# Kernel optimization log

Measured on AMD Instinct MI355X. Metric: run time of the kernel, lower is better.

Reference implementation:

```python
import jax, jax.numpy as jnp
import numpy as np

N = 100000
E = 1600000
IN_C, HID_C, OUT_C = 128, 128, 64


def setup_inputs() -> dict:
    key = jax.random.key(0)
    ks = jax.random.split(key, 8)
    x = jax.random.normal(ks[0], (N, IN_C), dtype=jnp.float32)
    edge_index = jax.random.randint(ks[1], (2, E), 0, N, dtype=jnp.int64)

    def glorot(k, fan_in, fan_out):
        s = jnp.sqrt(6.0 / (fan_in + fan_out))
        return jax.random.uniform(k, (fan_in, fan_out), jnp.float32, -s, s)

    W1 = glorot(ks[2], IN_C, HID_C)
    b1 = jnp.zeros((HID_C,), jnp.float32)
    W2 = glorot(ks[3], HID_C, HID_C)
    b2 = jnp.zeros((HID_C,), jnp.float32)
    W3 = glorot(ks[4], HID_C, OUT_C)
    b3 = jnp.zeros((OUT_C,), jnp.float32)
    return {"x": x, "edge_index": edge_index,
            "W1": W1, "b1": b1, "W2": W2, "b2": b2, "W3": W3, "b3": b3}


def _gcn_norm(row, col, n_nodes):
    # symmetric normalization, add_self_loops=False (PyG gcn_norm)
    deg = jax.ops.segment_sum(jnp.ones(row.shape[0], jnp.float32), col, num_segments=n_nodes)
    dinv = jnp.where(deg > 0, jax.lax.rsqrt(jnp.maximum(deg, 1.0)), 0.0)
    dinv = jnp.where(deg > 0, deg ** -0.5, 0.0)
    return dinv[row] * dinv[col]  # [E]


def _gcn_conv(x, row, col, norm, W, b):
    h = x @ W                                # [N, F_out] dense GEMM first (PyG order)
    msg = h[row] * norm[:, None]             # gather + scale, [E, F_out]
    out = jax.ops.segment_sum(msg, col, num_segments=x.shape[0])  # scatter-add
    return out + b


def reference(x, edge_index, W1, b1, W2, b2, W3, b3):
    row, col = edge_index[0], edge_index[1]
    norm = _gcn_norm(row, col, x.shape[0])
    h = jax.nn.relu(_gcn_conv(x, row, col, norm, W1, b1))   # dropout is identity in eval
    h = jax.nn.relu(_gcn_conv(h, row, col, norm, W2, b2))
    out = _gcn_conv(h, row, col, norm, W3, b3)
    return out
```

## Files before the change

kernel.cpp:

```cpp
#include <hip/hip_runtime.h>
#include <hip/hip_bf16.h>
#include <hip/hip_fp16.h>


#define K_DIM 128
#define SCAN_CHUNK 1024

typedef _Float16 f16x8 __attribute__((ext_vector_type(8)));
typedef float f32x4 __attribute__((ext_vector_type(4)));
struct h2s { _Float16 x, y; };

static inline long long cdiv_ll(long long a, long long b) { return (a + b - 1) / b; }

__global__ __launch_bounds__(256) void count_kernel(const int* __restrict__ col, int* __restrict__ cnt,
                                                    int* __restrict__ rank, int E) {
    int e = blockIdx.x * 256 + threadIdx.x;
    if (e < E) rank[e] = atomicAdd(&cnt[col[e]], 1);
}

__global__ __launch_bounds__(256) void dinv_kernel(const int* __restrict__ cnt, float* __restrict__ dinv, int N) {
    int n = blockIdx.x * 256 + threadIdx.x;
    if (n < N) {
        int d = cnt[n];
        dinv[n] = (d > 0) ? (1.0f / sqrtf((float)d)) : 0.0f;
    }
}

__global__ __launch_bounds__(256) void scan1_kernel(const int* __restrict__ cnt, int* __restrict__ off,
                                                    int* __restrict__ bsum, int N) {
    __shared__ int lds[256];
    const int t = threadIdx.x;
    const int base = blockIdx.x * SCAN_CHUNK;
    int v[4], s = 0;
#pragma unroll
    for (int j = 0; j < 4; ++j) {
        int i = base + t * 4 + j;
        v[j] = (i < N) ? cnt[i] : 0;
        s += v[j];
    }
    lds[t] = s;
    __syncthreads();
    for (int d = 1; d < 256; d <<= 1) {
        int x = (t >= d) ? lds[t - d] : 0;
        __syncthreads();
        lds[t] += x;
        __syncthreads();
    }
    int excl = lds[t] - s;
    if (t == 255) bsum[blockIdx.x] = lds[255];
    int run = excl;
#pragma unroll
    for (int j = 0; j < 4; ++j) {
        int i = base + t * 4 + j;
        if (i < N) off[i] = run;
        run += v[j];
    }
}

__global__ __launch_bounds__(256) void scan2_kernel(int* __restrict__ bsum, int G, int* __restrict__ off,
                                                    int N, int E) {
    __shared__ int lds[256];
    const int t = threadIdx.x;
    int s = (t < G) ? bsum[t] : 0;
    lds[t] = s;
    __syncthreads();
    for (int d = 1; d < 256; d <<= 1) {
        int x = (t >= d) ? lds[t - d] : 0;
        __syncthreads();
        lds[t] += x;
        __syncthreads();
    }
    if (t < G) bsum[t] = lds[t] - s;
    if (t == 0) off[N] = E;
}

__global__ __launch_bounds__(256) void scan3_kernel(int* __restrict__ off, const int* __restrict__ bsum, int N) {
    int add = bsum[blockIdx.x];
    const int base = blockIdx.x * SCAN_CHUNK;
#pragma unroll
    for (int j = 0; j < 4; ++j) {
        int i = base + threadIdx.x * 4 + j;
        if (i < N) off[i] += add;
    }
}

__global__ __launch_bounds__(256) void fill_kernel(const int* __restrict__ row, const int* __restrict__ col,
                                                   const int* __restrict__ off, const int* __restrict__ rank,
                                                   int* __restrict__ csr_row, int E) {
    int e = blockIdx.x * 256 + threadIdx.x;
    if (e < E) {
        int idx = off[col[e]] + rank[e];
        __builtin_nontemporal_store(row[e], &csr_row[idx]);
    }
}

template <int COUT>
__global__ __launch_bounds__(256) void pack_w_kernel(const float* __restrict__ W, _Float16* __restrict__ Wp) {
    constexpr int NT = COUT / 16;
    int t = blockIdx.x * 256 + threadIdx.x;
    if (t >= 4 * NT * 64) return;
    int lane = t & 63;
    int nt = (t >> 6) % NT;
    int kt = t / (64 * NT);
    int c = lane & 15, q = lane >> 4;
    f16x8 v;
#pragma unroll
    for (int j = 0; j < 8; ++j) {
        int k = kt * 32 + q * 8 + j;
        v[j] = (_Float16)W[k * COUT + nt * 16 + c];
    }
    *(f16x8*)&Wp[(size_t)t * 8] = v;
}

template <int COUT, bool AF16>
__global__ __launch_bounds__(256) void gemm_mfma(const void* __restrict__ Av, const _Float16* __restrict__ Wp,
                                                 const float* __restrict__ dinv, _Float16* __restrict__ Cmat, int M) {
    constexpr int NT = COUT / 16;
    constexpr int NFRAG = 4 * NT * 64;
    __shared__ _Float16 Wlds[NFRAG * 8];

    const int t = threadIdx.x;
    for (int i = t; i < NFRAG; i += 256)
        *(f16x8*)&Wlds[(size_t)i * 8] = *(const f16x8*)&Wp[(size_t)i * 8];
    __syncthreads();

    const int lane = t & 63;
    const int wave = t >> 6;
    const int c = lane & 15;
    const int q = lane >> 4;
    const int row_base = blockIdx.x * 128 + wave * 32;

    f32x4 acc[2][NT];
#pragma unroll
    for (int rt = 0; rt < 2; ++rt)
#pragma unroll
        for (int nt = 0; nt < NT; ++nt) {
            acc[rt][nt][0] = 0.f; acc[rt][nt][1] = 0.f;
            acc[rt][nt][2] = 0.f; acc[rt][nt][3] = 0.f;
        }

#pragma unroll
    for (int kt = 0; kt < 4; ++kt) {
        f16x8 a[2];
#pragma unroll
        for (int rt = 0; rt < 2; ++rt) {
            int r = row_base + rt * 16 + c;
            r = (r < M) ? r : (M - 1);
            if (AF16) {
                const _Float16* Ap = (const _Float16*)Av;
                int p = kt * 2 + (q >> 1);
                a[rt] = *(const f16x8*)&Ap[((size_t)p * M + r) * 16 + (q & 1) * 8];
            } else {
                const float* ap = (const float*)Av + (size_t)r * K_DIM + kt * 32 + q * 8;
                float4 v0 = *(const float4*)ap;
                float4 v1 = *(const float4*)(ap + 4);
                f16x8 av;
                av[0] = (_Float16)v0.x; av[1] = (_Float16)v0.y;
                av[2] = (_Float16)v0.z; av[3] = (_Float16)v0.w;
                av[4] = (_Float16)v1.x; av[5] = (_Float16)v1.y;
                av[6] = (_Float16)v1.z; av[7] = (_Float16)v1.w;
                a[rt] = av;
            }
        }
#pragma unroll
        for (int nt = 0; nt < NT; ++nt) {
            f16x8 b = *(const f16x8*)&Wlds[(size_t)((kt * NT + nt) * 64 + lane) * 8];
            acc[0][nt] = __builtin_amdgcn_mfma_f32_16x16x32_f16(a[0], b, acc[0][nt], 0, 0, 0);
            acc[1][nt] = __builtin_amdgcn_mfma_f32_16x16x32_f16(a[1], b, acc[1][nt], 0, 0, 0);
        }
    }

#pragma unroll
    for (int rt = 0; rt < 2; ++rt)
#pragma unroll
        for (int reg = 0; reg < 4; ++reg) {
            int row = row_base + rt * 16 + q * 4 + reg;
            if (row < M) {
                float dv = dinv[row];
#pragma unroll
                for (int nt = 0; nt < NT; ++nt)
                    Cmat[((size_t)nt * M + row) * 16 + c] = (_Float16)(acc[rt][nt][reg] * dv);
            }
        }
}

template <int NP, bool RELU, typename OutT>
__global__ __launch_bounds__(256) void gather_lds(const _Float16* __restrict__ g, const int* __restrict__ off,
                                                  const int* __restrict__ csr_row, const float* __restrict__ dinv,
                                                  const float* __restrict__ bias, OutT* __restrict__ outp, int N) {
    constexpr int NTILE = 32;
    constexpr int CH = 512;
    __shared__ _Float16 feat[CH * 16];
    __shared__ int off_s[NTILE + 1];

    const int t = threadIdx.x;
    const int plane = blockIdx.x % NP;
    const int node0 = (blockIdx.x / NP) * NTILE;
    const _Float16* gp = g + (size_t)plane * N * 16;

    if (t <= NTILE) {
        int idx = node0 + t;
        off_s[t] = off[idx < N ? idx : N];
    }
    __syncthreads();

    const int n_loc = t >> 3;
    const int q = t & 7;
    const int node = node0 + n_loc;
    const bool valid = node < N;
    const int sn0 = off_s[n_loc];
    const int sn1 = off_s[n_loc + 1];
    const int s_begin = off_s[0];
    const int s_end = off_s[NTILE];

    float ax = 0.f, ay = 0.f;

    for (int cs = s_begin; cs < s_end; cs += CH) {
        const int ce = (cs + CH < s_end) ? (cs + CH) : s_end;
        const int cnt = ce - cs;
        for (int i = t; i < cnt; i += 256) {
            int r = csr_row[cs + i];
            const _Float16* src = gp + (size_t)r * 16;
            f16x8 lo = *(const f16x8*)src;
            f16x8 hi = *(const f16x8*)(src + 8);
            *(f16x8*)&feat[i * 16] = lo;
            *(f16x8*)&feat[i * 16 + 8] = hi;
        }
        __syncthreads();
        const int lo_s = (sn0 > cs) ? sn0 : cs;
        const int hi_s = (sn1 < ce) ? sn1 : ce;
        for (int s = lo_s; s < hi_s; ++s) {
            h2s v = *(const h2s*)&feat[(s - cs) * 16 + q * 2];
            ax += (float)v.x;
            ay += (float)v.y;
        }
        __syncthreads();
    }

    if (valid) {
        float dv = dinv[node];
        float ox = ax * dv + bias[plane * 16 + q * 2 + 0];
        float oy = ay * dv + bias[plane * 16 + q * 2 + 1];
        if (RELU) { ox = fmaxf(ox, 0.f); oy = fmaxf(oy, 0.f); }
        if constexpr (sizeof(OutT) == 2) {
            h2s o; o.x = (_Float16)ox; o.y = (_Float16)oy;
            *(h2s*)((_Float16*)outp + ((size_t)plane * N + node) * 16 + q * 2) = o;
        } else {
            float2 o = make_float2(ox, oy);
            *(float2*)((float*)outp + (size_t)node * 64 + plane * 16 + q * 2) = o;
        }
    }
}

extern "C" void kernel_launch(void* const* d_in, const int* in_sizes, int n_in,
                              void* d_out, int out_size, void* d_ws, size_t ws_size,
                              hipStream_t stream) {
    const float* x  = (const float*)d_in[0];
    const int*   ei = (const int*)d_in[1];
    const float* W1 = (const float*)d_in[2];
    const float* b1 = (const float*)d_in[3];
    const float* W2 = (const float*)d_in[4];
    const float* b2 = (const float*)d_in[5];
    const float* W3 = (const float*)d_in[6];
    const float* b3 = (const float*)d_in[7];

    const int N = in_sizes[0] / 128;
    const int E = in_sizes[1] / 2;
    const int* row = ei;
    const int* col = ei + E;
    const int G = (int)cdiv_ll(N, SCAN_CHUNK);

    char* wsb = (char*)d_ws;
    int*      cnt     = (int*)wsb;      wsb += (size_t)N * 4;
    float*    dinv    = (float*)wsb;    wsb += (size_t)N * 4;
    int*      off     = (int*)wsb;      wsb += (size_t)(N + 1) * 4;
    int*      bsum    = (int*)wsb;      wsb += 256 * 4;
    int*      rank    = (int*)wsb;      wsb += (size_t)E * 4;
    int*      csr_row = (int*)wsb;      wsb += (size_t)E * 4;
    wsb = (char*)((((uintptr_t)wsb) + 15) & ~(uintptr_t)15);
    _Float16* Wp1     = (_Float16*)wsb; wsb += 16384 * 2;
    _Float16* Wp2     = (_Float16*)wsb; wsb += 16384 * 2;
    _Float16* Wp3     = (_Float16*)wsb; wsb += 8192 * 2;
    _Float16* bufA    = (_Float16*)wsb; wsb += (size_t)N * 128 * 2;
    _Float16* bufB    = (_Float16*)wsb;
    float*    out     = (float*)d_out;

    hipMemsetAsync(cnt, 0, (size_t)N * 4, stream);
    count_kernel<<<cdiv_ll(E, 256), 256, 0, stream>>>(col, cnt, rank, E);
    dinv_kernel<<<cdiv_ll(N, 256), 256, 0, stream>>>(cnt, dinv, N);
    scan1_kernel<<<G, 256, 0, stream>>>(cnt, off, bsum, N);
    scan2_kernel<<<1, 256, 0, stream>>>(bsum, G, off, N, E);
    scan3_kernel<<<G, 256, 0, stream>>>(off, bsum, N);
    fill_kernel<<<cdiv_ll(E, 256), 256, 0, stream>>>(row, col, off, rank, csr_row, E);
    pack_w_kernel<128><<<8, 256, 0, stream>>>(W1, Wp1);
    pack_w_kernel<128><<<8, 256, 0, stream>>>(W2, Wp2);
    pack_w_kernel<64><<<4, 256, 0, stream>>>(W3, Wp3);

    const long long gemmBlocks = cdiv_ll(N, 128);
    const long long nb         = cdiv_ll(N, 32);

    gemm_mfma<128, false><<<gemmBlocks, 256, 0, stream>>>(x, Wp1, dinv, bufA, N);
    gather_lds<8, true, _Float16><<<nb * 8, 256, 0, stream>>>(bufA, off, csr_row, dinv, b1, bufB, N);

    gemm_mfma<128, true><<<gemmBlocks, 256, 0, stream>>>(bufB, Wp2, dinv, bufA, N);
    gather_lds<8, true, _Float16><<<nb * 8, 256, 0, stream>>>(bufA, off, csr_row, dinv, b2, bufB, N);

    gemm_mfma<64, true><<<gemmBlocks, 256, 0, stream>>>(bufB, Wp3, dinv, bufA, N);
    gather_lds<4, false, float><<<nb * 4, 256, 0, stream>>>(bufA, off, csr_row, dinv, b3, out, N);
}
```

Before: 492.2 us.

## Switch intermediate features from plane-split to row-major layout with full-row gathers

```diff
diff --git a/kernel.cpp b/kernel.cpp
--- a/kernel.cpp
+++ b/kernel.cpp
@@ -8,7 +8,6 @@
 
 typedef _Float16 f16x8 __attribute__((ext_vector_type(8)));
 typedef float f32x4 __attribute__((ext_vector_type(4)));
-struct h2s { _Float16 x, y; };
 
 static inline long long cdiv_ll(long long a, long long b) { return (a + b - 1) / b; }
 
@@ -147,9 +146,7 @@
             int r = row_base + rt * 16 + c;
             r = (r < M) ? r : (M - 1);
             if (AF16) {
-                const _Float16* Ap = (const _Float16*)Av;
-                int p = kt * 2 + (q >> 1);
-                a[rt] = *(const f16x8*)&Ap[((size_t)p * M + r) * 16 + (q & 1) * 8];
+                a[rt] = *(const f16x8*)((const _Float16*)Av + (size_t)r * K_DIM + kt * 32 + q * 8);
             } else {
                 const float* ap = (const float*)Av + (size_t)r * K_DIM + kt * 32 + q * 8;
                 float4 v0 = *(const float4*)ap;
@@ -179,24 +176,25 @@
                 float dv = dinv[row];
 #pragma unroll
                 for (int nt = 0; nt < NT; ++nt)
-                    Cmat[((size_t)nt * M + row) * 16 + c] = (_Float16)(acc[rt][nt][reg] * dv);
+                    Cmat[(size_t)row * COUT + nt * 16 + c] = (_Float16)(acc[rt][nt][reg] * dv);
             }
         }
 }
 
-template <int NP, bool RELU, typename OutT>
-__global__ __launch_bounds__(256) void gather_lds(const _Float16* __restrict__ g, const int* __restrict__ off,
+template <int C, bool RELU, typename OutT>
+__global__ __launch_bounds__(256) void gather_row(const _Float16* __restrict__ g, const int* __restrict__ off,
                                                   const int* __restrict__ csr_row, const float* __restrict__ dinv,
                                                   const float* __restrict__ bias, OutT* __restrict__ outp, int N) {
-    constexpr int NTILE = 32;
-    constexpr int CH = 512;
-    __shared__ _Float16 feat[CH * 16];
+    constexpr int SUBS = C / 8;
+    constexpr int LOG_SUBS = (SUBS == 16) ? 4 : 3;
+    constexpr int NTILE = 256 / SUBS;
+    constexpr int CH = 96;
+    constexpr int RST = C + 8;
+    __shared__ __align__(16) _Float16 feat[CH * RST];
     __shared__ int off_s[NTILE + 1];
 
     const int t = threadIdx.x;
-    const int plane = blockIdx.x % NP;
-    const int node0 = (blockIdx.x / NP) * NTILE;
-    const _Float16* gp = g + (size_t)plane * N * 16;
+    const int node0 = blockIdx.x * NTILE;
 
     if (t <= NTILE) {
         int idx = node0 + t;
@@ -204,8 +202,8 @@
     }
     __syncthreads();
 
-    const int n_loc = t >> 3;
-    const int q = t & 7;
+    const int n_loc = t >> LOG_SUBS;
+    const int sub = t & (SUBS - 1);
     const int node = node0 + n_loc;
     const bool valid = node < N;
     const int sn0 = off_s[n_loc];
@@ -213,41 +211,51 @@
     const int s_begin = off_s[0];
     const int s_end = off_s[NTILE];
 
-    float ax = 0.f, ay = 0.f;
+    float acc[8];
+#pragma unroll
+    for (int k = 0; k < 8; ++k) acc[k] = 0.f;
 
     for (int cs = s_begin; cs < s_end; cs += CH) {
         const int ce = (cs + CH < s_end) ? (cs + CH) : s_end;
         const int cnt = ce - cs;
-        for (int i = t; i < cnt; i += 256) {
-            int r = csr_row[cs + i];
-            const _Float16* src = gp + (size_t)r * 16;
-            f16x8 lo = *(const f16x8*)src;
-            f16x8 hi = *(const f16x8*)(src + 8);
-            *(f16x8*)&feat[i * 16] = lo;
-            *(f16x8*)&feat[i * 16 + 8] = hi;
+        const int units = cnt << LOG_SUBS;
+        for (int u = t; u < units; u += 256) {
+            int rloc = u >> LOG_SUBS;
+            int seg = u & (SUBS - 1);
+            int r = csr_row[cs + rloc];
+            f16x8 v = *(const f16x8*)(g + (size_t)r * C + seg * 8);
+            *(f16x8*)&feat[rloc * RST + seg * 8] = v;
         }
         __syncthreads();
         const int lo_s = (sn0 > cs) ? sn0 : cs;
         const int hi_s = (sn1 < ce) ? sn1 : ce;
+        const _Float16* fb = &feat[sub * 8];
         for (int s = lo_s; s < hi_s; ++s) {
-            h2s v = *(const h2s*)&feat[(s - cs) * 16 + q * 2];
-            ax += (float)v.x;
-            ay += (float)v.y;
+            f16x8 v = *(const f16x8*)&fb[(s - cs) * RST];
+#pragma unroll
+            for (int k = 0; k < 8; ++k) acc[k] += (float)v[k];
         }
         __syncthreads();
     }
 
     if (valid) {
-        float dv = dinv[node];
-        float ox = ax * dv + bias[plane * 16 + q * 2 + 0];
-        float oy = ay * dv + bias[plane * 16 + q * 2 + 1];
-        if (RELU) { ox = fmaxf(ox, 0.f); oy = fmaxf(oy, 0.f); }
+        const float dv = dinv[node];
+        const float* bp = bias + sub * 8;
+        float o[8];
+#pragma unroll
+        for (int k = 0; k < 8; ++k) {
+            o[k] = acc[k] * dv + bp[k];
+            if (RELU) o[k] = fmaxf(o[k], 0.f);
+        }
         if constexpr (sizeof(OutT) == 2) {
-            h2s o; o.x = (_Float16)ox; o.y = (_Float16)oy;
-            *(h2s*)((_Float16*)outp + ((size_t)plane * N + node) * 16 + q * 2) = o;
+            f16x8 ov;
+#pragma unroll
+            for (int k = 0; k < 8; ++k) ov[k] = (_Float16)o[k];
+            *(f16x8*)((_Float16*)outp + (size_t)node * C + sub * 8) = ov;
         } else {
-            float2 o = make_float2(ox, oy);
-            *(float2*)((float*)outp + (size_t)node * 64 + plane * 16 + q * 2) = o;
+            float* op = (float*)outp + (size_t)node * C + sub * 8;
+            *(float4*)op = make_float4(o[0], o[1], o[2], o[3]);
+            *(float4*)(op + 4) = make_float4(o[4], o[5], o[6], o[7]);
         }
     }
 }
@@ -297,14 +305,15 @@
     pack_w_kernel<64><<<4, 256, 0, stream>>>(W3, Wp3);
 
     const long long gemmBlocks = cdiv_ll(N, 128);
-    const long long nb         = cdiv_ll(N, 32);
+    const long long g128Blocks = cdiv_ll(N, 16);
+    const long long g64Blocks  = cdiv_ll(N, 32);
 
     gemm_mfma<128, false><<<gemmBlocks, 256, 0, stream>>>(x, Wp1, dinv, bufA, N);
-    gather_lds<8, true, _Float16><<<nb * 8, 256, 0, stream>>>(bufA, off, csr_row, dinv, b1, bufB, N);
+    gather_row<128, true, _Float16><<<g128Blocks, 256, 0, stream>>>(bufA, off, csr_row, dinv, b1, bufB, N);
 
     gemm_mfma<128, true><<<gemmBlocks, 256, 0, stream>>>(bufB, Wp2, dinv, bufA, N);
-    gather_lds<8, true, _Float16><<<nb * 8, 256, 0, stream>>>(bufA, off, csr_row, dinv, b2, bufB, N);
+    gather_row<128, true, _Float16><<<g128Blocks, 256, 0, stream>>>(bufA, off, csr_row, dinv, b2, bufB, N);
 
     gemm_mfma<64, true><<<gemmBlocks, 256, 0, stream>>>(bufB, Wp3, dinv, bufA, N);
-    gather_lds<4, false, float><<<nb * 4, 256, 0, stream>>>(bufA, off, csr_row, dinv, b3, out, N);
-}
+    gather_row<64, false, float><<<g64Blocks, 256, 0, stream>>>(bufA, off, csr_row, dinv, b3, out, N);
+}
```

Measured after the change: 520.2 us. +5.7%, slower.
